# Performance work log

Measured on AMD Instinct MI355X. Metric: run time of the kernel, lower is better.

## Reference

```python
import jax, jax.numpy as jnp
import numpy as np

N = 50000       # nodes per subgraph scale
E = 800000      # edges per subgraph scale
B = 4096        # number of subgraphs (graphs in the batch)
IN, HID, OUT = 64, 64, 32
NE = 8          # num_experts
EMB = 64        # emb_dim per expert
E2 = 131072     # graph-level edges for distortion loss


def setup_inputs() -> dict:
    key = jax.random.key(0)
    ks = jax.random.split(key, 16)
    inv = lambda d: 1.0 / np.sqrt(d)
    return {
        "subgraph_x0": jax.random.normal(ks[0], (N, IN), jnp.float32),
        "subgraph_x1": jax.random.normal(ks[1], (N, IN), jnp.float32),
        "W1": jax.random.normal(ks[2], (IN, HID), jnp.float32) * inv(IN),
        "b1": jnp.zeros((HID,), jnp.float32),
        "W2": jax.random.normal(ks[3], (HID, OUT), jnp.float32) * inv(HID),
        "b2": jnp.zeros((OUT,), jnp.float32),
        "Wc": jax.random.normal(ks[4], (OUT * 2, NE), jnp.float32) * inv(OUT * 2),
        "bc": jnp.zeros((NE,), jnp.float32),
        "embeddings": jax.random.normal(ks[5], (B, NE * EMB), jnp.float32),
        # precomputed shortest-path distances per graph edge (positive)
        "dis": jax.random.uniform(ks[6], (E2,), jnp.float32) * 1.5 + 0.5,
        "edge_index0": jax.random.randint(ks[7], (2, E), 0, N, jnp.int32),
        "edge_index1": jax.random.randint(ks[8], (2, E), 0, N, jnp.int32),
        "batch0": jnp.sort(jax.random.randint(ks[9], (N,), 0, B, jnp.int32)),
        "batch1": jnp.sort(jax.random.randint(ks[10], (N,), 0, B, jnp.int32)),
        "edge_index2": jax.random.randint(ks[11], (2, E2), 0, B, jnp.int32),
        "emb_dim": EMB,
    }


def _gcn_conv(x, W, b, src, dst, n):
    """PyG GCNConv: D^{-1/2}(A+I)D^{-1/2} X W + b, with self-loops."""
    xw = x @ W  # [n, out]
    ones = jnp.ones(src.shape, xw.dtype)
    deg = jax.ops.segment_sum(ones, dst, num_segments=n) + 1.0  # self-loop degree
    dinv = jax.lax.rsqrt(deg)  # [n]
    norm = dinv[src] * dinv[dst]  # [E]
    agg = jax.ops.segment_sum(xw[src] * norm[:, None], dst, num_segments=n)
    agg = agg + (dinv * dinv)[:, None] * xw  # self-loop messages
    return agg + b


def _mean_pool(x, batch, num_graphs):
    s = jax.ops.segment_sum(x, batch, num_segments=num_graphs)
    cnt = jax.ops.segment_sum(jnp.ones((x.shape[0],), x.dtype), batch,
                              num_segments=num_graphs)
    return s / jnp.maximum(cnt, 1.0)[:, None]


def _encode_scale(x, edge_index, batch, W1, b1, W2, b2, num_graphs):
    src, dst = edge_index[0], edge_index[1]
    n = x.shape[0]
    h = _gcn_conv(x, W1, b1, src, dst, n)
    h = _gcn_conv(h, W2, b2, src, dst, n)
    return _mean_pool(h, batch, num_graphs)


def reference(subgraph_x0, subgraph_x1, W1, b1, W2, b2, Wc, bc,
              embeddings, dis, edge_index0, edge_index1,
              batch0, batch1, edge_index2, emb_dim):
    num_graphs = embeddings.shape[0]
    x0 = _encode_scale(subgraph_x0, edge_index0, batch0, W1, b1, W2, b2, num_graphs)
    x1 = _encode_scale(subgraph_x1, edge_index1, batch1, W1, b1, W2, b2, num_graphs)
    x = jnp.concatenate([x0, x1], axis=-1)  # [B, 2*OUT]
    gate = jax.nn.softmax(x @ Wc + bc, axis=-1)  # temperature = 1.0

    # distortion loss over graph-level edges
    s, d = edge_index2[0], edge_index2[1]
    e = edge_index2.shape[1]
    diff = (embeddings[s] - embeddings[d]) ** 2  # [E2, NE*emb_dim]
    diff = diff.reshape(e, diff.shape[1] // emb_dim, emb_dim).sum(axis=2)  # [E2, NE]
    weights = jax.nn.softmax(gate[s] * gate[d], axis=1)  # [E2, NE]
    dsum = jnp.sum(diff * weights, axis=-1)  # [E2]
    loss_distortion = jnp.mean(jnp.abs(dsum / dis - 1.0))
    return gate, loss_distortion
```

## Files before the change

kernel.cpp:

```cpp
#include <hip/hip_runtime.h>
#include <math.h>

constexpr int IN_F  = 64;
constexpr int HID_F = 64;
constexpr int OUT_F = 32;
constexpr int NEXP  = 8;
constexpr int EMB   = 64;


__global__ void zero_f32_kernel(float* __restrict__ p, long long n) {
    long long i = (long long)blockIdx.x * blockDim.x + threadIdx.x;
    long long stride = (long long)gridDim.x * blockDim.x;
    for (; i < n; i += stride) p[i] = 0.0f;
}

__global__ void zero_i32_kernel(int* __restrict__ p, long long n) {
    long long i = (long long)blockIdx.x * blockDim.x + threadIdx.x;
    long long stride = (long long)gridDim.x * blockDim.x;
    for (; i < n; i += stride) p[i] = 0;
}

__global__ __launch_bounds__(1024)
void w12_kernel(const float* __restrict__ W1, const float* __restrict__ W2,
                const float* __restrict__ b1,
                float* __restrict__ W12, float* __restrict__ c1)
{
    __shared__ float sW2[HID_F * OUT_F];
    const int tid = threadIdx.x;
    for (int i = tid; i < HID_F * OUT_F; i += 1024) sW2[i] = W2[i];
    __syncthreads();
    for (int idx = tid; idx < IN_F * OUT_F; idx += 1024) {
        int i = idx >> 5, j = idx & 31;
        float acc = 0.0f;
#pragma unroll
        for (int k = 0; k < HID_F; ++k) acc += W1[i * HID_F + k] * sW2[k * OUT_F + j];
        W12[idx] = acc;
    }
    if (tid < OUT_F) {
        float acc = 0.0f;
#pragma unroll
        for (int k = 0; k < HID_F; ++k) acc += b1[k] * sW2[k * OUT_F + tid];
        c1[tid] = acc;
    }
}

__global__ void hist2_kernel(const int* __restrict__ ei0, const int* __restrict__ ei1,
                             int* __restrict__ counts, int E, int N)
{
    int e = blockIdx.x * blockDim.x + threadIdx.x;
    if (e >= 2 * E) return;
    int d = (e < E) ? ei0[E + e] : (ei1[E + (e - E)] + N);
    atomicAdd(&counts[d], 1);
}

__global__ __launch_bounds__(1024)
void scan1_kernel(const int* __restrict__ counts, int* __restrict__ lexcl,
                  int* __restrict__ partials, int N)
{
    __shared__ int wsum[16];
    const int tid  = threadIdx.x;
    const int lane = tid & 63;
    const int wv   = tid >> 6;
    const int i    = blockIdx.x * 1024 + tid;

    int v = (i < N) ? counts[i] : 0;
    int x = v;
#pragma unroll
    for (int off = 1; off < 64; off <<= 1) {
        int t = __shfl_up(x, off);
        if (lane >= off) x += t;
    }
    if (lane == 63) wsum[wv] = x;
    __syncthreads();
    int woff = 0;
    for (int w = 0; w < wv; ++w) woff += wsum[w];
    if (i < N) lexcl[i] = woff + x - v;
    if (tid == 1023) partials[blockIdx.x] = woff + x;
}

__global__ __launch_bounds__(1024)
void scan2_kernel(int* __restrict__ partials, int NB)
{
    __shared__ int wsum[16];
    const int tid  = threadIdx.x;
    const int lane = tid & 63;
    const int wv   = tid >> 6;
    int v = (tid < NB) ? partials[tid] : 0;
    int x = v;
#pragma unroll
    for (int off = 1; off < 64; off <<= 1) {
        int t = __shfl_up(x, off);
        if (lane >= off) x += t;
    }
    if (lane == 63) wsum[wv] = x;
    __syncthreads();
    int woff = 0;
    for (int w = 0; w < wv; ++w) woff += wsum[w];
    if (tid < NB) partials[tid] = woff + x - v;
}

__global__ void scan3_kernel(const int* __restrict__ lexcl, const int* __restrict__ partials,
                             const int* __restrict__ counts,
                             int* __restrict__ offsets, int* __restrict__ cursor,
                             float* __restrict__ dinv, int n2, int e2tot)
{
    int i = blockIdx.x * blockDim.x + threadIdx.x;
    if (i >= n2) return;
    int o = lexcl[i] + partials[i >> 10];
    offsets[i] = o;
    cursor[i]  = o;
    dinv[i] = rsqrtf((float)counts[i] + 1.0f);
    if (i == 0) offsets[n2] = e2tot;
}

__global__ __launch_bounds__(256)
void scatter2_shard_kernel(const int* __restrict__ ei0, const int* __restrict__ ei1,
                           int* __restrict__ cursor, int* __restrict__ csr_src,
                           int E, int N, int n2)
{
    const int shard   = blockIdx.x & 7;
    const int bid     = blockIdx.x >> 3;
    const int nblocks = gridDim.x >> 3;
    const int lo = (int)(((long long)n2 * shard) >> 3);
    const int hi = (int)(((long long)n2 * (shard + 1)) >> 3);

    long long start  = (long long)bid * blockDim.x + threadIdx.x;
    long long stride = (long long)nblocks * blockDim.x;
    const long long e2 = 2LL * E;
    for (long long e = start; e < e2; e += stride) {
        int s, d;
        if (e < E) { s = ei0[e];                 d = ei0[E + e]; }
        else       { s = ei1[e - E] + N;         d = ei1[E + (e - E)] + N; }
        if (d >= lo && d < hi) {
            int pos = atomicAdd(&cursor[d], 1);
            csr_src[pos] = s;
        }
    }
}

__global__ __launch_bounds__(256)
void gemm_ys2_kernel(const float* __restrict__ x0, const float* __restrict__ x1,
                     const float* __restrict__ W12, const float* __restrict__ dinv,
                     float* __restrict__ Ys, int N, int n2)
{
    __shared__ float Ws[IN_F * OUT_F];
    __shared__ float xs[8 * IN_F];
    const int tid = threadIdx.x;

    for (int i = tid; i < IN_F * OUT_F; i += 256) Ws[i] = W12[i];
    const int row0 = blockIdx.x * 8;
    for (int i = tid; i < 8 * IN_F; i += 256) {
        int r = i >> 6;
        int rr = row0 + r;
        float v = 0.0f;
        if (rr < n2) {
            v = (rr < N) ? x0[(size_t)rr * IN_F + (i & 63)]
                         : x1[(size_t)(rr - N) * IN_F + (i & 63)];
        }
        xs[i] = v;
    }
    __syncthreads();

    const int r = tid >> 5;
    const int c = tid & 31;
    const int row = row0 + r;
    if (row >= n2) return;

    float acc = 0.0f;
#pragma unroll
    for (int k = 0; k < IN_F; ++k) acc += xs[r * IN_F + k] * Ws[k * OUT_F + c];

    Ys[(size_t)row * OUT_F + c] = acc * dinv[row];
}

template<int MODE>
__global__ __launch_bounds__(256)
void csr_agg32_kernel(const int* __restrict__ csr_src, const int* __restrict__ offsets,
                      const float* __restrict__ in, const float* __restrict__ dinv,
                      float* __restrict__ sdsum, const float* __restrict__ c1,
                      const float* __restrict__ b2,
                      float* __restrict__ out, int n)
{
    constexpr int F = OUT_F;
    const int lane = threadIdx.x & 63;
    const int wid  = (blockIdx.x * (blockDim.x >> 6)) + (threadIdx.x >> 6);
    const int sub  = lane >> 5;
    const int f    = lane & 31;
    const int node = wid * 2 + sub;
    const int lbase = sub * F;

    const bool valid = (node < n);
    const int nc   = valid ? node : 0;
    const int off0 = offsets[nc];
    const int off1 = valid ? offsets[nc + 1] : off0;

    float acc0 = valid ? in[(size_t)nc * F + f] : 0.0f;
    float acc1 = 0.0f, acc2 = 0.0f, acc3 = 0.0f;
    float dsum = 0.0f;
    for (int k = off0; k < off1; k += F) {
        int nk = off1 - k; if (nk > F) nk = F;
        int sj = (f < nk) ? csr_src[k + f] : 0;
        if (MODE == 0) {
            float dv = dinv[sj];
            dsum += (f < nk) ? dv : 0.0f;
        }
        int t = 0;
        for (; t + 8 <= nk; t += 8) {
            int s0 = __shfl(sj, lbase + t);
            int s1 = __shfl(sj, lbase + t + 1);
            int s2 = __shfl(sj, lbase + t + 2);
            int s3 = __shfl(sj, lbase + t + 3);
            int s4 = __shfl(sj, lbase + t + 4);
            int s5 = __shfl(sj, lbase + t + 5);
            int s6 = __shfl(sj, lbase + t + 6);
            int s7 = __shfl(sj, lbase + t + 7);
            float v0 = in[(size_t)s0 * F + f];
            float v1 = in[(size_t)s1 * F + f];
            float v2 = in[(size_t)s2 * F + f];
            float v3 = in[(size_t)s3 * F + f];
            float v4 = in[(size_t)s4 * F + f];
            float v5 = in[(size_t)s5 * F + f];
            float v6 = in[(size_t)s6 * F + f];
            float v7 = in[(size_t)s7 * F + f];
            acc0 += v0 + v4;
            acc1 += v1 + v5;
            acc2 += v2 + v6;
            acc3 += v3 + v7;
        }
        for (; t < nk; ++t) {
            int s = __shfl(sj, lbase + t);
            acc0 += in[(size_t)s * F + f];
        }
    }
    if (MODE == 0) {
#pragma unroll
        for (int off = 1; off < 32; off <<= 1) dsum += __shfl_xor(dsum, off);
    }
    if (valid) {
        float di = dinv[node];
        float s = (acc0 + acc1) + (acc2 + acc3);
        if (MODE == 0) {
            out[(size_t)node * F + f] = di * di * s;
            if (f == 0) sdsum[node] = dsum;
        } else {
            float t = di * (di + sdsum[node]);
            out[(size_t)node * F + f] = di * s + t * c1[f] + b2[f];
        }
    }
}

__global__ void pool_sum2_kernel(const float* __restrict__ h,
                                 const int* __restrict__ bat0, const int* __restrict__ bat1,
                                 float* __restrict__ pooled, float* __restrict__ cnt,
                                 int N, int n2, int B)
{
    int t = blockIdx.x * blockDim.x + threadIdx.x;
    int i = t >> 5;
    int f = t & 31;
    if (i >= n2) return;
    int g = (i < N) ? bat0[i] : (bat1[i - N] + B);
    atomicAdd(&pooled[(size_t)g * OUT_F + f], h[(size_t)i * OUT_F + f]);
    if (f == 0) atomicAdd(&cnt[g], 1.0f);
}

__global__ void pool_div_kernel(float* __restrict__ pooled, const float* __restrict__ cnt, int B2)
{
    int t = blockIdx.x * blockDim.x + threadIdx.x;
    if (t >= B2 * OUT_F) return;
    int g = t >> 5;
    pooled[t] /= fmaxf(cnt[g], 1.0f);
}

__global__ void gate_kernel(const float* __restrict__ p0, const float* __restrict__ p1,
                            const float* __restrict__ Wc, const float* __restrict__ bc,
                            float* __restrict__ gate, int B)
{
    int g = blockIdx.x * blockDim.x + threadIdx.x;
    if (g >= B) return;
    float xv[2 * OUT_F];
#pragma unroll
    for (int k = 0; k < OUT_F; ++k) xv[k] = p0[(size_t)g * OUT_F + k];
#pragma unroll
    for (int k = 0; k < OUT_F; ++k) xv[OUT_F + k] = p1[(size_t)g * OUT_F + k];

    float lg[NEXP];
    float m = -1e30f;
#pragma unroll
    for (int e = 0; e < NEXP; ++e) {
        float acc = bc[e];
#pragma unroll
        for (int k = 0; k < 2 * OUT_F; ++k) acc += xv[k] * Wc[k * NEXP + e];
        lg[e] = acc;
        m = fmaxf(m, acc);
    }
    float se = 0.0f;
#pragma unroll
    for (int e = 0; e < NEXP; ++e) { lg[e] = expf(lg[e] - m); se += lg[e]; }
    float inv = 1.0f / se;
#pragma unroll
    for (int e = 0; e < NEXP; ++e) gate[(size_t)g * NEXP + e] = lg[e] * inv;
}

__global__ void zero_scalar_kernel(float* p) { *p = 0.0f; }

__global__ void histK_kernel(const int* __restrict__ s_idx, const int* __restrict__ d_idx,
                             int* __restrict__ histK, int E2, int B, int quarter)
{
    int e = blockIdx.x * blockDim.x + threadIdx.x;
    if (e >= E2) return;
    int qd = d_idx[e] / quarter; if (qd > 3) qd = 3;
    atomicAdd(&histK[qd * B + s_idx[e]], 1);
}

__global__ void combineK_kernel(const int* __restrict__ lexclK, const int* __restrict__ partialsK,
                                int* __restrict__ offK, int* __restrict__ curK, int nk, int E2)
{
    int i = blockIdx.x * blockDim.x + threadIdx.x;
    if (i >= nk) return;
    int o = lexclK[i] + partialsK[i >> 10];
    offK[i] = o;
    curK[i] = o;
    if (i == 0) offK[nk] = E2;
}

__global__ void scatterK_kernel(const int* __restrict__ s_idx, const int* __restrict__ d_idx,
                                const float* __restrict__ dis,
                                int* __restrict__ curK, int* __restrict__ dD,
                                float* __restrict__ disD, int E2, int B, int quarter)
{
    int e = blockIdx.x * blockDim.x + threadIdx.x;
    if (e >= E2) return;
    int d = d_idx[e];
    int qd = d / quarter; if (qd > 3) qd = 3;
    int pos = atomicAdd(&curK[qd * B + s_idx[e]], 1);
    dD[pos] = d;
    disD[pos] = dis[e];
}

__global__ __launch_bounds__(256)
void distortion6_kernel(const float* __restrict__ emb, const float* __restrict__ gate,
                        const int* __restrict__ offK, const int* __restrict__ dD,
                        const float* __restrict__ disD,
                        float* __restrict__ loss, int B, int E2)
{
    const int lane = threadIdx.x & 63;
    const int q    = lane >> 4;
    const int ql   = lane & 15;
    const int xcd  = blockIdx.x & 7;
    const int bid  = blockIdx.x >> 3;
    const int wv   = threadIdx.x >> 6;
    const int wIdx = bid * 4 + wv;
    const int nws  = (gridDim.x >> 3) * 4;

    const int qd   = xcd >> 1;
    const int sh   = xcd & 1;
    const int halfB = B >> 1;
    const int k0 = qd * B + sh * halfB;
    const int k1 = qd * B + (sh ? B : halfB);

    const float4* emb4  = (const float4*)emb;
    const float4* gate4 = (const float4*)gate;

    float lsum = 0.0f;
    for (int k = k0 + wIdx; k < k1; k += nws) {
        const int j0 = offK[k];
        const int j1 = offK[k + 1];
        if (j0 == j1) continue;
        const int s = k - qd * B;

        const float4* es = emb4 + (size_t)s * 128;
        float4 a0 = es[ql];
        float4 a1 = es[ql + 16];
        float4 a2 = es[ql + 32];
        float4 a3 = es[ql + 48];
        float4 a4 = es[ql + 64];
        float4 a5 = es[ql + 80];
        float4 a6 = es[ql + 96];
        float4 a7 = es[ql + 112];
        float4 gs0 = gate4[(size_t)s * 2];
        float4 gs1 = gate4[(size_t)s * 2 + 1];

        for (int j = j0 + q; j < j1; j += 4) {
            int d = dD[j];
            float dv = disD[j];
            const float4* ed = emb4 + (size_t)d * 128;
            float4 b0 = ed[ql];
            float4 b1 = ed[ql + 16];
            float4 b2 = ed[ql + 32];
            float4 b3 = ed[ql + 48];
            float4 b4 = ed[ql + 64];
            float4 b5 = ed[ql + 80];
            float4 b6 = ed[ql + 96];
            float4 b7 = ed[ql + 112];
            float4 gd0 = gate4[(size_t)d * 2];
            float4 gd1 = gate4[(size_t)d * 2 + 1];

            float p[NEXP];
            float dx;
            dx = a0.x - b0.x; p[0]  = dx * dx;
            dx = a0.y - b0.y; p[0] += dx * dx;
            dx = a0.z - b0.z; p[0] += dx * dx;
            dx = a0.w - b0.w; p[0] += dx * dx;
            dx = a1.x - b1.x; p[1]  = dx * dx;
            dx = a1.y - b1.y; p[1] += dx * dx;
            dx = a1.z - b1.z; p[1] += dx * dx;
            dx = a1.w - b1.w; p[1] += dx * dx;
            dx = a2.x - b2.x; p[2]  = dx * dx;
            dx = a2.y - b2.y; p[2] += dx * dx;
            dx = a2.z - b2.z; p[2] += dx * dx;
            dx = a2.w - b2.w; p[2] += dx * dx;
            dx = a3.x - b3.x; p[3]  = dx * dx;
            dx = a3.y - b3.y; p[3] += dx * dx;
            dx = a3.z - b3.z; p[3] += dx * dx;
            dx = a3.w - b3.w; p[3] += dx * dx;
            dx = a4.x - b4.x; p[4]  = dx * dx;
            dx = a4.y - b4.y; p[4] += dx * dx;
            dx = a4.z - b4.z; p[4] += dx * dx;
            dx = a4.w - b4.w; p[4] += dx * dx;
            dx = a5.x - b5.x; p[5]  = dx * dx;
            dx = a5.y - b5.y; p[5] += dx * dx;
            dx = a5.z - b5.z; p[5] += dx * dx;
            dx = a5.w - b5.w; p[5] += dx * dx;
            dx = a6.x - b6.x; p[6]  = dx * dx;
            dx = a6.y - b6.y; p[6] += dx * dx;
            dx = a6.z - b6.z; p[6] += dx * dx;
            dx = a6.w - b6.w; p[6] += dx * dx;
            dx = a7.x - b7.x; p[7]  = dx * dx;
            dx = a7.y - b7.y; p[7] += dx * dx;
            dx = a7.z - b7.z; p[7] += dx * dx;
            dx = a7.w - b7.w; p[7] += dx * dx;

#pragma unroll
            for (int off = 1; off < 16; off <<= 1) {
#pragma unroll
                for (int t = 0; t < NEXP; ++t) p[t] += __shfl_xor(p[t], off);
            }

            float gp[NEXP] = { gs0.x * gd0.x, gs0.y * gd0.y, gs0.z * gd0.z, gs0.w * gd0.w,
                               gs1.x * gd1.x, gs1.y * gd1.y, gs1.z * gd1.z, gs1.w * gd1.w };
            float m = gp[0];
#pragma unroll
            for (int t = 1; t < NEXP; ++t) m = fmaxf(m, gp[t]);
            float se = 0.0f;
#pragma unroll
            for (int t = 0; t < NEXP; ++t) { gp[t] = expf(gp[t] - m); se += gp[t]; }
            float dsum = 0.0f;
#pragma unroll
            for (int t = 0; t < NEXP; ++t) dsum += p[t] * gp[t];

            lsum += fabsf((dsum / se) / dv - 1.0f);
        }
    }
    lsum += __shfl_xor(lsum, 16);
    lsum += __shfl_xor(lsum, 32);
    if (lane == 0) atomicAdd(loss, lsum / (float)E2);
}

extern "C" void kernel_launch(void* const* d_in, const int* in_sizes, int n_in,
                              void* d_out, int out_size, void* d_ws, size_t ws_size,
                              hipStream_t stream)
{
    const float* x0   = (const float*)d_in[0];
    const float* x1   = (const float*)d_in[1];
    const float* W1   = (const float*)d_in[2];
    const float* b1   = (const float*)d_in[3];
    const float* W2   = (const float*)d_in[4];
    const float* b2   = (const float*)d_in[5];
    const float* Wc   = (const float*)d_in[6];
    const float* bc   = (const float*)d_in[7];
    const float* emb  = (const float*)d_in[8];
    const float* dis  = (const float*)d_in[9];
    const int*   ei0  = (const int*)d_in[10];
    const int*   ei1  = (const int*)d_in[11];
    const int*   bat0 = (const int*)d_in[12];
    const int*   bat1 = (const int*)d_in[13];
    const int*   ei2  = (const int*)d_in[14];

    const int N  = in_sizes[0] / IN_F;
    const int E  = in_sizes[10] / 2;
    const int B  = in_sizes[8] / (NEXP * EMB);
    const int E2 = in_sizes[14] / 2;
    const int n2 = 2 * N;
    const int nk = 4 * B;
    const int quarter = (B + 3) / 4;

    float* gate_out = (float*)d_out;
    float* loss_out = gate_out + (size_t)B * NEXP;

    float* ws      = (float*)d_ws;
    float* dinv    = ws;
    float* Ys      = dinv + n2;
    float* Zs      = Ys + (size_t)n2 * OUT_F;
    float* sdsum   = Zs + (size_t)n2 * OUT_F;
    float* pooled  = sdsum + n2;
    float* cnt     = pooled + (size_t)2 * B * OUT_F;
    float* W12     = cnt + 2 * B;
    float* c1      = W12 + IN_F * OUT_F;
    float* disD    = c1 + OUT_F;
    int*   iws     = (int*)(disD + E2);
    int*   counts  = iws;
    int*   offsets = counts + n2;
    int*   cursor  = offsets + n2 + 1;
    int*   csr_src = cursor + n2;
    int*   lexcl   = csr_src + 2 * E;
    int*   partials= lexcl + n2;
    int*   histK   = partials + 1024;
    int*   lexclK  = histK + nk;
    int*   partialsK = lexclK + nk;
    int*   offK    = partialsK + 1024;
    int*   curK    = offK + nk + 1;
    int*   dD      = curK + nk;

    const int TB = 256;
    const int zgrid = 512;
    const int NB2 = (n2 + 1023) / 1024;
    const int NBK = (nk + 1023) / 1024;

    w12_kernel<<<1, 1024, 0, stream>>>(W1, W2, b1, W12, c1);

    zero_i32_kernel<<<zgrid, TB, 0, stream>>>(counts, n2);
    hist2_kernel<<<(2 * E + TB - 1) / TB, TB, 0, stream>>>(ei0, ei1, counts, E, N);
    scan1_kernel<<<NB2, 1024, 0, stream>>>(counts, lexcl, partials, n2);
    scan2_kernel<<<1, 1024, 0, stream>>>(partials, NB2);
    scan3_kernel<<<(n2 + TB - 1) / TB, TB, 0, stream>>>(lexcl, partials, counts,
                                                        offsets, cursor, dinv, n2, 2 * E);
    scatter2_shard_kernel<<<1024, TB, 0, stream>>>(ei0, ei1, cursor, csr_src, E, N, n2);

    zero_i32_kernel<<<zgrid, TB, 0, stream>>>(histK, nk);
    histK_kernel<<<(E2 + TB - 1) / TB, TB, 0, stream>>>(ei2, ei2 + E2, histK, E2, B, quarter);
    scan1_kernel<<<NBK, 1024, 0, stream>>>(histK, lexclK, partialsK, nk);
    scan2_kernel<<<1, 1024, 0, stream>>>(partialsK, NBK);
    combineK_kernel<<<(nk + TB - 1) / TB, TB, 0, stream>>>(lexclK, partialsK, offK, curK, nk, E2);
    scatterK_kernel<<<(E2 + TB - 1) / TB, TB, 0, stream>>>(ei2, ei2 + E2, dis,
                                                           curK, dD, disD, E2, B, quarter);

    gemm_ys2_kernel<<<(n2 + 7) / 8, 256, 0, stream>>>(x0, x1, W12, dinv, Ys, N, n2);
    csr_agg32_kernel<0><<<(n2 + 7) / 8, TB, 0, stream>>>(csr_src, offsets, Ys, dinv,
                                                         sdsum, nullptr, nullptr, Zs, n2);
    csr_agg32_kernel<1><<<(n2 + 7) / 8, TB, 0, stream>>>(csr_src, offsets, Zs, dinv,
                                                         sdsum, c1, b2, Ys, n2);

    zero_f32_kernel<<<zgrid, TB, 0, stream>>>(pooled, (long long)2 * B * OUT_F);
    zero_f32_kernel<<<zgrid, TB, 0, stream>>>(cnt, 2 * B);
    pool_sum2_kernel<<<((n2 * 32) + TB - 1) / TB, TB, 0, stream>>>(Ys, bat0, bat1,
                                                                   pooled, cnt, N, n2, B);
    pool_div_kernel<<<((2 * B * OUT_F) + TB - 1) / TB, TB, 0, stream>>>(pooled, cnt, 2 * B);

    gate_kernel<<<(B + TB - 1) / TB, TB, 0, stream>>>(pooled, pooled + (size_t)B * OUT_F,
                                                      Wc, bc, gate_out, B);

    zero_scalar_kernel<<<1, 1, 0, stream>>>(loss_out);
    distortion6_kernel<<<1024, TB, 0, stream>>>(emb, gate_out, offK, dD, disD,
                                                loss_out, B, E2);
}
```

Measured before the change: 407.7 us.

## Replace 8-shard edge rescans with a two-phase bucket partition before CSR scatter

The old scatter kernel made every edge be read by all eight shard groups, filtering by destination range. Now edges are first counted per shard and appended into per-shard buckets with wave-aggregated atomics (ballot, popcount, leader atomic). Each shard then scatters only its own bucket into the CSR. This removes the eightfold re-reading of the edge arrays but adds three extra launches and an intermediate int2 buffer that reuses the Ys workspace.

```diff
diff --git a/kernel.cpp b/kernel.cpp
--- a/kernel.cpp
+++ b/kernel.cpp
@@ -114,27 +114,84 @@
 }
 
 __global__ __launch_bounds__(256)
-void scatter2_shard_kernel(const int* __restrict__ ei0, const int* __restrict__ ei1,
-                           int* __restrict__ cursor, int* __restrict__ csr_src,
-                           int E, int N, int n2)
+void shard_hist_kernel(const int* __restrict__ ei0, const int* __restrict__ ei1,
+                       int* __restrict__ bCnt, int E, int N, int n2)
+{
+    __shared__ int h[8];
+    if (threadIdx.x < 8) h[threadIdx.x] = 0;
+    __syncthreads();
+    long long e = (long long)blockIdx.x * blockDim.x + threadIdx.x;
+    long long stride = (long long)gridDim.x * blockDim.x;
+    const long long e2 = 2LL * E;
+    for (; e < e2; e += stride) {
+        int d = (e < E) ? ei0[E + e] : (ei1[E + (e - E)] + N);
+        int sh = (int)((8LL * d) / n2);
+        atomicAdd(&h[sh], 1);
+    }
+    __syncthreads();
+    if (threadIdx.x < 8) atomicAdd(&bCnt[threadIdx.x], h[threadIdx.x]);
+}
+
+__global__ void scan8_kernel(const int* __restrict__ bCnt, int* __restrict__ bOff,
+                             int* __restrict__ bCur)
+{
+    if (threadIdx.x == 0) {
+        int acc = 0;
+        for (int i = 0; i < 8; ++i) { bOff[i] = acc; bCur[i] = acc; acc += bCnt[i]; }
+        bOff[8] = acc;
+    }
+}
+
+__global__ __launch_bounds__(256)
+void bucket_append_kernel(const int* __restrict__ ei0, const int* __restrict__ ei1,
+                          int* __restrict__ bCur, int2* __restrict__ bucket,
+                          int E, int N, int n2)
+{
+    const int lane = threadIdx.x & 63;
+    const long long stride = (long long)gridDim.x * blockDim.x;
+    const long long e2 = 2LL * E;
+    for (long long bb = (long long)blockIdx.x * blockDim.x; bb < e2; bb += stride) {
+        long long e = bb + threadIdx.x;
+        bool valid = (e < e2);
+        int s = 0, d = 0, sh = -1;
+        if (valid) {
+            if (e < E) { s = ei0[e];             d = ei0[E + e]; }
+            else       { s = ei1[e - E] + N;     d = ei1[E + (e - E)] + N; }
+            sh = (int)((8LL * d) / n2);
+        }
+#pragma unroll
+        for (int b = 0; b < 8; ++b) {
+            unsigned long long mask = __ballot(valid && sh == b);
+            if (mask == 0ull) continue;
+            int cnt = __popcll(mask);
+            int leader = __ffsll((unsigned long long)mask) - 1;
+            int base = 0;
+            if (lane == leader) base = atomicAdd(&bCur[b], cnt);
+            base = __shfl(base, leader);
+            if (valid && sh == b) {
+                unsigned long long lt = (lane == 0) ? 0ull
+                                       : (~0ull >> (64 - lane));
+                int off = __popcll(mask & lt);
+                bucket[base + off] = make_int2(d, s);
+            }
+        }
+    }
+}
+
+__global__ __launch_bounds__(256)
+void scatter_phase2_kernel(const int2* __restrict__ bucket, const int* __restrict__ bOff,
+                           int* __restrict__ cursor, int* __restrict__ csr_src)
 {
     const int shard   = blockIdx.x & 7;
     const int bid     = blockIdx.x >> 3;
     const int nblocks = gridDim.x >> 3;
-    const int lo = (int)(((long long)n2 * shard) >> 3);
-    const int hi = (int)(((long long)n2 * (shard + 1)) >> 3);
-
-    long long start  = (long long)bid * blockDim.x + threadIdx.x;
-    long long stride = (long long)nblocks * blockDim.x;
-    const long long e2 = 2LL * E;
-    for (long long e = start; e < e2; e += stride) {
-        int s, d;
-        if (e < E) { s = ei0[e];                 d = ei0[E + e]; }
-        else       { s = ei1[e - E] + N;         d = ei1[E + (e - E)] + N; }
-        if (d >= lo && d < hi) {
-            int pos = atomicAdd(&cursor[d], 1);
-            csr_src[pos] = s;
-        }
+    const int j0 = bOff[shard];
+    const int j1 = bOff[shard + 1];
+    for (int j = j0 + bid * blockDim.x + threadIdx.x; j < j1;
+         j += nblocks * blockDim.x) {
+        int2 ed = bucket[j];
+        int pos = atomicAdd(&cursor[ed.x], 1);
+        csr_src[pos] = ed.y;
     }
 }
 
@@ -510,6 +567,10 @@
     int*   offK    = partialsK + 1024;
     int*   curK    = offK + nk + 1;
     int*   dD      = curK + nk;
+    int*   bCnt    = dD + E2;
+    int*   bOff    = bCnt + 8;
+    int*   bCur    = bOff + 9;
+    int2*  bucket  = (int2*)Ys;
 
     const int TB = 256;
     const int zgrid = 512;
@@ -519,12 +580,16 @@
     w12_kernel<<<1, 1024, 0, stream>>>(W1, W2, b1, W12, c1);
 
     zero_i32_kernel<<<zgrid, TB, 0, stream>>>(counts, n2);
+    zero_i32_kernel<<<1, 64, 0, stream>>>(bCnt, 8);
     hist2_kernel<<<(2 * E + TB - 1) / TB, TB, 0, stream>>>(ei0, ei1, counts, E, N);
     scan1_kernel<<<NB2, 1024, 0, stream>>>(counts, lexcl, partials, n2);
     scan2_kernel<<<1, 1024, 0, stream>>>(partials, NB2);
     scan3_kernel<<<(n2 + TB - 1) / TB, TB, 0, stream>>>(lexcl, partials, counts,
                                                         offsets, cursor, dinv, n2, 2 * E);
-    scatter2_shard_kernel<<<1024, TB, 0, stream>>>(ei0, ei1, cursor, csr_src, E, N, n2);
+    shard_hist_kernel<<<512, TB, 0, stream>>>(ei0, ei1, bCnt, E, N, n2);
+    scan8_kernel<<<1, 64, 0, stream>>>(bCnt, bOff, bCur);
+    bucket_append_kernel<<<512, TB, 0, stream>>>(ei0, ei1, bCur, bucket, E, N, n2);
+    scatter_phase2_kernel<<<1024, TB, 0, stream>>>(bucket, bOff, cursor, csr_src);
 
     zero_i32_kernel<<<zgrid, TB, 0, stream>>>(histK, nk);
     histK_kernel<<<(E2 + TB - 1) / TB, TB, 0, stream>>>(ei2, ei2 + E2, histK, E2, B, quarter);
```

New measurement: 1.555 ms. 282% more time.
